# Kernel optimization log

Measured on AMD Instinct MI355X. Metric: run time of the kernel, lower is better.

## Reference

```python
import jax, jax.numpy as jnp
import numpy as np

N_EMB, D_LAT, D_HID, D_MID, D_IN = 1024, 64, 256, 128, 9
BETA = 0.25  # commitment_cost
N = 262144


def _kaiming(k, shape):
    # kaiming_normal_ with nonlinearity='relu': std = sqrt(2 / fan_in)
    fan_in = shape[1]
    return jax.random.normal(k, shape, jnp.float32) * jnp.sqrt(jnp.float32(2.0 / fan_in))


def setup_inputs() -> dict:
    key = jax.random.key(0)
    ks = jax.random.split(key, 8)
    return {
        "x": jax.random.normal(ks[0], (N, D_IN), jnp.float32),
        # Encoder: Linear(9->256) ReLU Linear(256->128) ReLU Linear(128->64)
        "enc_w1": _kaiming(ks[1], (D_HID, D_IN)),  "enc_b1": jnp.zeros((D_HID,), jnp.float32),
        "enc_w2": _kaiming(ks[2], (D_MID, D_HID)), "enc_b2": jnp.zeros((D_MID,), jnp.float32),
        "enc_w3": _kaiming(ks[3], (D_LAT, D_MID)), "enc_b3": jnp.zeros((D_LAT,), jnp.float32),
        # Decoder: Linear(64->128) ReLU Linear(128->256) ReLU Linear(256->9)
        "dec_w1": _kaiming(ks[4], (D_MID, D_LAT)), "dec_b1": jnp.zeros((D_MID,), jnp.float32),
        "dec_w2": _kaiming(ks[5], (D_HID, D_MID)), "dec_b2": jnp.zeros((D_HID,), jnp.float32),
        "dec_w3": _kaiming(ks[6], (D_IN, D_HID)),  "dec_b3": jnp.zeros((D_IN,), jnp.float32),
        # Codebook: Embedding(1024, 64), uniform(-1, 1)
        "codebook": jax.random.uniform(ks[7], (N_EMB, D_LAT), jnp.float32, -1.0, 1.0),
    }


def _mlp3(h, w1, b1, w2, b2, w3, b3):
    h = jax.nn.relu(h @ w1.T + b1)
    h = jax.nn.relu(h @ w2.T + b2)
    return h @ w3.T + b3


def reference(x, enc_w1, enc_b1, enc_w2, enc_b2, enc_w3, enc_b3,
              dec_w1, dec_b1, dec_w2, dec_b2, dec_w3, dec_b3, codebook):
    z_e = _mlp3(x, enc_w1, enc_b1, enc_w2, enc_b2, enc_w3, enc_b3)  # [N, 64]
    # squared euclidean distances to codebook: [N, N_EMB]
    d = (jnp.sum(z_e * z_e, axis=1, keepdims=True)
         - 2.0 * (z_e @ codebook.T)
         + jnp.sum(codebook * codebook, axis=1))
    idx = jnp.argmin(d, axis=1)                 # [N] int
    quantized = codebook[idx]                   # gather == onehot @ codebook
    e_latent = jnp.mean((jax.lax.stop_gradient(quantized) - z_e) ** 2)
    q_latent = jnp.mean((quantized - jax.lax.stop_gradient(z_e)) ** 2)
    vq_loss = q_latent + BETA * e_latent
    # straight-through estimator
    z_q = z_e + jax.lax.stop_gradient(quantized - z_e)
    # perplexity from codebook usage histogram (== mean of one-hot encodings)
    counts = jnp.zeros((N_EMB,), jnp.float32).at[idx].add(1.0)
    avg_probs = counts / jnp.float32(z_e.shape[0])
    perplexity = jnp.exp(-jnp.sum(avg_probs * jnp.log(avg_probs + 1e-10)))
    x_recon = _mlp3(z_q, dec_w1, dec_b1, dec_w2, dec_b2, dec_w3, dec_b3)
    return (x_recon, vq_loss, perplexity)
```

## Files before the change

kernel.cpp:

```cpp
#include <hip/hip_runtime.h>
#include <math.h>


namespace {

constexpr int kN = 262144;

typedef _Float16 half8 __attribute__((ext_vector_type(8)));
typedef float floatx4 __attribute__((ext_vector_type(4)));

#define MFMA16(a, b, c) __builtin_amdgcn_mfma_f32_16x16x32_f16((a), (b), (c), 0, 0, 0)
#define LDS_FENCE() asm volatile("s_waitcnt lgkmcnt(0)" ::: "memory")
#define VMCNT0() asm volatile("s_waitcnt vmcnt(0)" ::: "memory")
#define BARRIER()                                  \
  do {                                             \
    asm volatile("" ::: "memory");                 \
    __builtin_amdgcn_s_barrier();                  \
    asm volatile("" ::: "memory");                 \
  } while (0)

constexpr size_t W1M_O = 0;
constexpr size_t W1R_O = 16384;
constexpr size_t E2M_O = 32768;
constexpr size_t E2R_O = 98304;
constexpr size_t E3M_O = 163840;
constexpr size_t E3R_O = 180224;
constexpr size_t CBM_O = 196608;
constexpr size_t CBR_O = 327680;
constexpr size_t D1P_O = 458752;
constexpr size_t D2P_O = 475136;
constexpr size_t D3P_O = 540672;
constexpr size_t CN_O  = 548864;
constexpr size_t IDX_O = 589824;
constexpr size_t ESP_O = IDX_O + 1048576;
constexpr size_t HP_O  = ESP_O + 32768;

__device__ __forceinline__ void split2(float v, _Float16& hi, _Float16& lo) {
  hi = (_Float16)v;
  lo = (_Float16)(v - (float)hi);
}

__global__ void prep_kernel(
    const float* __restrict__ ew1, const float* __restrict__ ew2,
    const float* __restrict__ ew3, const float* __restrict__ cb,
    const float* __restrict__ dw1, const float* __restrict__ dw2,
    const float* __restrict__ dw3, char* __restrict__ wsb) {
  _Float16* w1m = (_Float16*)(wsb + W1M_O);
  _Float16* w1r = (_Float16*)(wsb + W1R_O);
  _Float16* e2m = (_Float16*)(wsb + E2M_O);
  _Float16* e2r = (_Float16*)(wsb + E2R_O);
  _Float16* e3m = (_Float16*)(wsb + E3M_O);
  _Float16* e3r = (_Float16*)(wsb + E3R_O);
  _Float16* cbm = (_Float16*)(wsb + CBM_O);
  _Float16* cbr = (_Float16*)(wsb + CBR_O);
  _Float16* d1p = (_Float16*)(wsb + D1P_O);
  _Float16* d2p = (_Float16*)(wsb + D2P_O);
  _Float16* d3p = (_Float16*)(wsb + D3P_O);
  float* cn = (float*)(wsb + CN_O);

  const int gid = blockIdx.x * 256 + threadIdx.x;
  const int stride = gridDim.x * 256;
  for (int e = gid; e < 256 * 32; e += stride) {
    int n = e >> 5, k = e & 31;
    float v = (k < 9) ? ew1[n * 9 + k] : 0.f;
    split2(v, w1m[e], w1r[e]);
  }
  for (int e = gid; e < 128 * 256; e += stride) split2(ew2[e], e2m[e], e2r[e]);
  for (int e = gid; e < 64 * 128; e += stride) split2(ew3[e], e3m[e], e3r[e]);
  for (int e = gid; e < 1024 * 64; e += stride) split2(cb[e], cbm[e], cbr[e]);
  for (int e = gid; e < 128 * 64; e += stride) d1p[e] = (_Float16)dw1[e];
  for (int e = gid; e < 256 * 128; e += stride) d2p[e] = (_Float16)dw2[e];
  for (int e = gid; e < 16 * 256; e += stride) {
    int n = e >> 8, k = e & 255;
    d3p[e] = (n < 9) ? (_Float16)dw3[n * 256 + k] : (_Float16)0.f;
  }
  for (int i = gid; i < 1024; i += stride) {
    float s = 0.f;
    const float* c = cb + (size_t)i * 64;
#pragma unroll 8
    for (int k = 0; k < 64; ++k) s = fmaf(c[k], c[k], s);
    cn[i] = s;
  }
}

__global__ __launch_bounds__(256, 3) void vqvae_mega(
    const float* __restrict__ x,
    const float* __restrict__ eb1, const float* __restrict__ eb2,
    const float* __restrict__ eb3, const float* __restrict__ db1,
    const float* __restrict__ db2, const float* __restrict__ db3,
    const float* __restrict__ cb, const char* __restrict__ wsb,
    float* __restrict__ out, int* __restrict__ idx_g, float* __restrict__ esp_g) {
  __shared__ _Float16 LP[26624];

  const int t = threadIdx.x;
  const int lane = t & 63;
  const int w = t >> 6;
  const int m = lane & 15;
  const int q = lane >> 4;
  const int R0 = blockIdx.x * 128;
  const int wr0 = 32 * w;
  _Float16* WPS = LP + 16384 + w * 2560;
  const float* cn_g = (const float*)(wsb + CN_O);
  const int swq = (m & 7) << 3;

  half8 axm[2] = {{}, {}}, axr[2] = {{}, {}};
#pragma unroll
  for (int rt = 0; rt < 2; ++rt) {
    const int grow = R0 + wr0 + 16 * rt + m;
    if (q == 0) {
#pragma unroll
      for (int j = 0; j < 8; ++j) {
        const float v = x[(size_t)grow * 9 + j];
        const _Float16 hi = (_Float16)v;
        axm[rt][j] = hi;
        axr[rt][j] = (_Float16)(v - (float)hi);
      }
    } else if (q == 1) {
      const float v = x[(size_t)grow * 9 + 8];
      const _Float16 hi = (_Float16)v;
      axm[rt][0] = hi;
      axr[rt][0] = (_Float16)(v - (float)hi);
    }
  }

  floatx4 acc2[8][2];
#pragma unroll
  for (int nt = 0; nt < 8; ++nt)
#pragma unroll
    for (int rt = 0; rt < 2; ++rt) acc2[nt][rt] = (floatx4){0.f, 0.f, 0.f, 0.f};

  {
    const int pA = t >> 7, nA = t & 127;
    const char* srcA = wsb + (pA ? E2R_O : E2M_O) + (size_t)nA * 512;
    _Float16* dstA = LP + (pA ? 5120 : 0) + nA * 40;
    half8 stg[4];
#pragma unroll
    for (int j = 0; j < 4; ++j) stg[j] = *(const half8*)(srcA + j * 16);

    for (int kc = 0; kc < 8; ++kc) {
      VMCNT0();
#pragma unroll
      for (int j = 0; j < 4; ++j) *(half8*)(dstA + j * 8) = stg[j];
      LDS_FENCE();
      if (kc < 7) {
#pragma unroll
        for (int j = 0; j < 4; ++j)
          stg[j] = *(const half8*)(srcA + (size_t)(kc + 1) * 64 + j * 16);
      }
      BARRIER();

#pragma unroll
      for (int ntl = 0; ntl < 2; ++ntl) {
        const int f = kc * 32 + ntl * 16 + m;
        const half8 bm = *(const half8*)(wsb + W1M_O + (size_t)f * 64 + q * 16);
        const half8 br = *(const half8*)(wsb + W1R_O + (size_t)f * 64 + q * 16);
        const float bias = eb1[f];
#pragma unroll
        for (int rt = 0; rt < 2; ++rt) {
          floatx4 a = (floatx4){0.f, 0.f, 0.f, 0.f};
          a = MFMA16(axr[rt], bm, a);
          a = MFMA16(axm[rt], br, a);
          a = MFMA16(axm[rt], bm, a);
#pragma unroll
          for (int reg = 0; reg < 4; ++reg) {
            const float v = fmaxf(a[reg] + bias, 0.f);
            const int row = 16 * rt + 4 * q + reg;
            const _Float16 hi = (_Float16)v;
            WPS[row * 40 + ntl * 16 + m] = hi;
            WPS[1280 + row * 40 + ntl * 16 + m] = (_Float16)(v - (float)hi);
          }
        }
      }
      LDS_FENCE();
      half8 am[2], ar[2];
#pragma unroll
      for (int rt = 0; rt < 2; ++rt) {
        am[rt] = *(const half8*)(WPS + (16 * rt + m) * 40 + q * 8);
        ar[rt] = *(const half8*)(WPS + 1280 + (16 * rt + m) * 40 + q * 8);
      }
      __builtin_amdgcn_s_setprio(1);
#pragma unroll
      for (int nt = 0; nt < 8; ++nt) {
        const half8 bm = *(const half8*)(LP + (nt * 16 + m) * 40 + q * 8);
        const half8 br = *(const half8*)(LP + 5120 + (nt * 16 + m) * 40 + q * 8);
#pragma unroll
        for (int rt = 0; rt < 2; ++rt) {
          acc2[nt][rt] = MFMA16(ar[rt], bm, acc2[nt][rt]);
          acc2[nt][rt] = MFMA16(am[rt], br, acc2[nt][rt]);
          acc2[nt][rt] = MFMA16(am[rt], bm, acc2[nt][rt]);
        }
      }
      __builtin_amdgcn_s_setprio(0);
      BARRIER();
    }
  }

  floatx4 acc3[4][2];
#pragma unroll
  for (int nt = 0; nt < 4; ++nt)
#pragma unroll
    for (int rt = 0; rt < 2; ++rt) acc3[nt][rt] = (floatx4){0.f, 0.f, 0.f, 0.f};

  for (int ks = 0; ks < 4; ++ks) {
#pragma unroll
    for (int h = 0; h < 2; ++h) {
      const int nt = 2 * ks + h;
      const float bias = eb2[nt * 16 + m];
#pragma unroll
      for (int rt = 0; rt < 2; ++rt) {
#pragma unroll
        for (int reg = 0; reg < 4; ++reg) {
          const float v = fmaxf(acc2[nt][rt][reg] + bias, 0.f);
          const int row = 16 * rt + 4 * q + reg;
          const _Float16 hi = (_Float16)v;
          WPS[row * 40 + h * 16 + m] = hi;
          WPS[1280 + row * 40 + h * 16 + m] = (_Float16)(v - (float)hi);
        }
      }
    }
    LDS_FENCE();
    half8 am[2], ar[2];
#pragma unroll
    for (int rt = 0; rt < 2; ++rt) {
      am[rt] = *(const half8*)(WPS + (16 * rt + m) * 40 + q * 8);
      ar[rt] = *(const half8*)(WPS + 1280 + (16 * rt + m) * 40 + q * 8);
    }
#pragma unroll
    for (int nt = 0; nt < 4; ++nt) {
      const half8 bm = *(const half8*)(wsb + E3M_O + (size_t)(nt * 16 + m) * 256 + ks * 64 + q * 16);
      const half8 br = *(const half8*)(wsb + E3R_O + (size_t)(nt * 16 + m) * 256 + ks * 64 + q * 16);
#pragma unroll
      for (int rt = 0; rt < 2; ++rt) {
        acc3[nt][rt] = MFMA16(ar[rt], bm, acc3[nt][rt]);
        acc3[nt][rt] = MFMA16(am[rt], br, acc3[nt][rt]);
        acc3[nt][rt] = MFMA16(am[rt], bm, acc3[nt][rt]);
      }
    }
  }

  const int pC = t >> 7, eC = t & 127;
  const int nC = eC >> 1, hC = eC & 1;
  const char* srcC = wsb + (pC ? CBR_O : CBM_O) + (size_t)nC * 128 + hC * 64;
  const int dCbase = pC * 4096 + nC * 64;
  const int swC = (nC & 7) << 3;
  half8 stgC[4];
#pragma unroll
  for (int j = 0; j < 4; ++j) stgC[j] = *(const half8*)(srcC + j * 16);

  half8 zfm[2][2], zfr[2][2];
#pragma unroll
  for (int rt = 0; rt < 2; ++rt) {
#pragma unroll
    for (int nt = 0; nt < 4; ++nt) {
      const float bias = eb3[nt * 16 + m];
#pragma unroll
      for (int reg = 0; reg < 4; ++reg) {
        const float v = acc3[nt][rt][reg] + bias;
        const int row = 4 * q + reg;
        const _Float16 hi = (_Float16)v;
        WPS[row * 72 + nt * 16 + m] = hi;
        WPS[1152 + row * 72 + nt * 16 + m] = (_Float16)(v - (float)hi);
      }
    }
    LDS_FENCE();
#pragma unroll
    for (int ks2 = 0; ks2 < 2; ++ks2) {
      zfm[rt][ks2] = *(const half8*)(WPS + m * 72 + ks2 * 32 + q * 8);
      zfr[rt][ks2] = *(const half8*)(WPS + 1152 + m * 72 + ks2 * 32 + q * 8);
    }
  }

  float bestd[2][4];
  int besti[2][4];
#pragma unroll
  for (int rt = 0; rt < 2; ++rt)
#pragma unroll
    for (int reg = 0; reg < 4; ++reg) { bestd[rt][reg] = 3.4e38f; besti[rt][reg] = 0; }

  for (int cc = 0; cc < 16; ++cc) {
    const int bb = (cc & 1) << 13;
    VMCNT0();
    {
      _Float16* d0 = LP + bb + dCbase;
#pragma unroll
      for (int j = 0; j < 4; ++j)
        *(half8*)(d0 + ((hC * 32 + j * 8) ^ swC)) = stgC[j];
    }
    LDS_FENCE();
    if (cc < 15) {
#pragma unroll
      for (int j = 0; j < 4; ++j)
        stgC[j] = *(const half8*)(srcC + (size_t)(cc + 1) * 8192 + j * 16);
    }
    BARRIER();

    floatx4 accd[4][2];
#pragma unroll
    for (int nt = 0; nt < 4; ++nt)
#pragma unroll
      for (int rt = 0; rt < 2; ++rt) accd[nt][rt] = (floatx4){0.f, 0.f, 0.f, 0.f};
    __builtin_amdgcn_s_setprio(1);
#pragma unroll
    for (int nt = 0; nt < 4; ++nt) {
#pragma unroll
      for (int ks2 = 0; ks2 < 2; ++ks2) {
        const int ko = (ks2 * 32 + q * 8) ^ swq;
        const half8 bm = *(const half8*)(LP + bb + (nt * 16 + m) * 64 + ko);
        const half8 br = *(const half8*)(LP + bb + 4096 + (nt * 16 + m) * 64 + ko);
#pragma unroll
        for (int rt = 0; rt < 2; ++rt) {
          accd[nt][rt] = MFMA16(zfr[rt][ks2], bm, accd[nt][rt]);
          accd[nt][rt] = MFMA16(zfm[rt][ks2], br, accd[nt][rt]);
          accd[nt][rt] = MFMA16(zfm[rt][ks2], bm, accd[nt][rt]);
        }
      }
    }
    __builtin_amdgcn_s_setprio(0);
#pragma unroll
    for (int nt = 0; nt < 4; ++nt) {
      const int code = cc * 64 + nt * 16 + m;
      const float cnv = cn_g[code];
#pragma unroll
      for (int rt = 0; rt < 2; ++rt) {
#pragma unroll
        for (int reg = 0; reg < 4; ++reg) {
          const float d = cnv - 2.f * accd[nt][rt][reg];
          if (d < bestd[rt][reg]) { bestd[rt][reg] = d; besti[rt][reg] = code; }
        }
      }
    }
  }
#pragma unroll
  for (int rt = 0; rt < 2; ++rt) {
#pragma unroll
    for (int reg = 0; reg < 4; ++reg) {
#pragma unroll
      for (int off = 1; off < 16; off <<= 1) {
        const float od = __shfl_xor(bestd[rt][reg], off, 16);
        const int oi = __shfl_xor(besti[rt][reg], off, 16);
        if (od < bestd[rt][reg] || (od == bestd[rt][reg] && oi < besti[rt][reg])) {
          bestd[rt][reg] = od; besti[rt][reg] = oi;
        }
      }
    }
  }
  if (m == 0) {
#pragma unroll
    for (int rt = 0; rt < 2; ++rt)
#pragma unroll
      for (int reg = 0; reg < 4; ++reg) {
        const int row = wr0 + 16 * rt + 4 * q + reg;
        idx_g[R0 + row] = besti[rt][reg];
      }
  }

  const int sl = ((m >> 2) << 4) | m;
  half8 zq[2][2];
  float es = 0.f;
#pragma unroll
  for (int rt = 0; rt < 2; ++rt) {
    const int b0 = __shfl(besti[rt][0], sl);
    const int b1 = __shfl(besti[rt][1], sl);
    const int b2 = __shfl(besti[rt][2], sl);
    const int b3 = __shfl(besti[rt][3], sl);
    const int r2 = m & 3;
    const int bi = (r2 == 0) ? b0 : (r2 == 1) ? b1 : (r2 == 2) ? b2 : b3;
#pragma unroll
    for (int ks2 = 0; ks2 < 2; ++ks2) {
      const float* cp = cb + (size_t)bi * 64 + ks2 * 32 + q * 8;
      const float4 c0 = *(const float4*)cp;
      const float4 c1 = *(const float4*)(cp + 4);
      float cv[8] = {c0.x, c0.y, c0.z, c0.w, c1.x, c1.y, c1.z, c1.w};
#pragma unroll
      for (int j = 0; j < 8; ++j) {
        const float z = (float)zfm[rt][ks2][j] + (float)zfr[rt][ks2][j];
        const float d = cv[j] - z;
        es = fmaf(d, d, es);
        zq[rt][ks2][j] = (_Float16)(z + d);
      }
    }
  }
#pragma unroll
  for (int off = 1; off < 64; off <<= 1) es += __shfl_xor(es, off, 64);
  if (lane == 0) esp_g[blockIdx.x * 4 + w] = es;

  const int nE = t >> 2, jE = t & 3;
  const char* srcE = wsb + D2P_O + (size_t)nE * 256 + jE * 64;
  const int dEbase = nE * 128;
  const int swE = (nE & 7) << 3;
  half8 stgE[4];
#pragma unroll
  for (int j = 0; j < 4; ++j) stgE[j] = *(const half8*)(srcE + j * 16);

  floatx4 accH[8][2];
#pragma unroll
  for (int nt = 0; nt < 8; ++nt)
#pragma unroll
    for (int rt = 0; rt < 2; ++rt) accH[nt][rt] = (floatx4){0.f, 0.f, 0.f, 0.f};
  __builtin_amdgcn_s_setprio(1);
#pragma unroll
  for (int nt = 0; nt < 8; ++nt) {
#pragma unroll
    for (int ks2 = 0; ks2 < 2; ++ks2) {
      const half8 b = *(const half8*)(wsb + D1P_O + (size_t)(nt * 16 + m) * 128 + ks2 * 64 + q * 16);
#pragma unroll
      for (int rt = 0; rt < 2; ++rt) accH[nt][rt] = MFMA16(zq[rt][ks2], b, accH[nt][rt]);
    }
  }
  __builtin_amdgcn_s_setprio(0);
  half8 h3f[2][4];
  for (int ks = 0; ks < 4; ++ks) {
#pragma unroll
    for (int h = 0; h < 2; ++h) {
      const int nt = 2 * ks + h;
      const float bias = db1[nt * 16 + m];
#pragma unroll
      for (int rt = 0; rt < 2; ++rt)
#pragma unroll
        for (int reg = 0; reg < 4; ++reg) {
          const float v = fmaxf(accH[nt][rt][reg] + bias, 0.f);
          WPS[(16 * rt + 4 * q + reg) * 40 + h * 16 + m] = (_Float16)v;
        }
    }
    LDS_FENCE();
#pragma unroll
    for (int rt = 0; rt < 2; ++rt)
      h3f[rt][ks] = *(const half8*)(WPS + (16 * rt + m) * 40 + q * 8);
  }

  floatx4 accO[2] = {(floatx4){0.f, 0.f, 0.f, 0.f}, (floatx4){0.f, 0.f, 0.f, 0.f}};
  for (int jc = 0; jc < 4; ++jc) {
    const int bb = (jc & 1) << 13;
    VMCNT0();
    {
      _Float16* d0 = LP + bb + dEbase;
#pragma unroll
      for (int j = 0; j < 4; ++j)
        *(half8*)(d0 + ((jE * 32 + j * 8) ^ swE)) = stgE[j];
    }
    LDS_FENCE();
    if (jc < 3) {
#pragma unroll
      for (int j = 0; j < 4; ++j)
        stgE[j] = *(const half8*)(srcE + (size_t)(jc + 1) * 16384 + j * 16);
    }
    BARRIER();

    floatx4 accD2[4][2];
#pragma unroll
    for (int nt = 0; nt < 4; ++nt)
#pragma unroll
      for (int rt = 0; rt < 2; ++rt) accD2[nt][rt] = (floatx4){0.f, 0.f, 0.f, 0.f};
    __builtin_amdgcn_s_setprio(1);
#pragma unroll
    for (int nt = 0; nt < 4; ++nt) {
#pragma unroll
      for (int ks = 0; ks < 4; ++ks) {
        const half8 b = *(const half8*)(LP + bb + (nt * 16 + m) * 128 + ((ks * 32 + q * 8) ^ swq));
#pragma unroll
        for (int rt = 0; rt < 2; ++rt) accD2[nt][rt] = MFMA16(h3f[rt][ks], b, accD2[nt][rt]);
      }
    }
    __builtin_amdgcn_s_setprio(0);
    half8 b3[2];
#pragma unroll
    for (int ks2 = 0; ks2 < 2; ++ks2)
      b3[ks2] = *(const half8*)(wsb + D3P_O + (size_t)m * 512 + jc * 128 + ks2 * 64 + q * 16);
#pragma unroll
    for (int rt = 0; rt < 2; ++rt) {
#pragma unroll
      for (int nt = 0; nt < 4; ++nt) {
        const float bias = db2[jc * 64 + nt * 16 + m];
#pragma unroll
        for (int reg = 0; reg < 4; ++reg) {
          const float v = fmaxf(accD2[nt][rt][reg] + bias, 0.f);
          WPS[(4 * q + reg) * 72 + nt * 16 + m] = (_Float16)v;
        }
      }
      LDS_FENCE();
#pragma unroll
      for (int ks2 = 0; ks2 < 2; ++ks2) {
        const half8 am = *(const half8*)(WPS + m * 72 + ks2 * 32 + q * 8);
        accO[rt] = MFMA16(am, b3[ks2], accO[rt]);
      }
    }
  }
  if (m < 9) {
    const float bias = db3[m];
#pragma unroll
    for (int rt = 0; rt < 2; ++rt)
#pragma unroll
      for (int reg = 0; reg < 4; ++reg) {
        const size_t r = (size_t)(R0 + wr0 + 16 * rt + 4 * q + reg);
        out[r * 9 + m] = accO[rt][reg] + bias;
      }
  }
}

__global__ __launch_bounds__(256) void hist_kernel(
    const int* __restrict__ idx_g, int* __restrict__ hp) {
  __shared__ int lh[1024];
  const int t = threadIdx.x;
#pragma unroll
  for (int i = 0; i < 4; ++i) lh[t * 4 + i] = 0;
  __syncthreads();
  for (int i = t; i < 4096; i += 256)
    atomicAdd(&lh[idx_g[blockIdx.x * 4096 + i]], 1);
  __syncthreads();
  int* part = hp + blockIdx.x * 1024;
#pragma unroll
  for (int i = 0; i < 4; ++i) part[t * 4 + i] = lh[t * 4 + i];
}

__global__ __launch_bounds__(1024) void finalize_kernel(
    const int* __restrict__ hp, const float* __restrict__ esp,
    float* __restrict__ out2) {
  __shared__ double red[1024];
  __shared__ float rede[1024];
  const int t = threadIdx.x;
  int h = 0;
#pragma unroll 8
  for (int p = 0; p < 64; ++p) h += hp[p * 1024 + t];
  const float pr = (float)h * (1.0f / (float)kN);
  red[t] = (double)(pr * logf(pr + 1e-10f));
  float es = 0.f;
#pragma unroll
  for (int i = 0; i < 8; ++i) es += esp[i * 1024 + t];
  rede[t] = es;
  __syncthreads();
  for (int s = 512; s > 0; s >>= 1) {
    if (t < s) { red[t] += red[t + s]; rede[t] += rede[t + s]; }
    __syncthreads();
  }
  if (t == 0) {
    out2[0] = 1.25f * (rede[0] * (1.0f / ((float)kN * 64.0f)));
    out2[1] = expf((float)(-red[0]));
  }
}

}

extern "C" void kernel_launch(void* const* d_in, const int* in_sizes, int n_in,
                              void* d_out, int out_size, void* d_ws, size_t ws_size,
                              hipStream_t stream) {
  const float* x   = (const float*)d_in[0];
  const float* ew1 = (const float*)d_in[1];
  const float* eb1 = (const float*)d_in[2];
  const float* ew2 = (const float*)d_in[3];
  const float* eb2 = (const float*)d_in[4];
  const float* ew3 = (const float*)d_in[5];
  const float* eb3 = (const float*)d_in[6];
  const float* dw1 = (const float*)d_in[7];
  const float* db1 = (const float*)d_in[8];
  const float* dw2 = (const float*)d_in[9];
  const float* db2 = (const float*)d_in[10];
  const float* dw3 = (const float*)d_in[11];
  const float* db3 = (const float*)d_in[12];
  const float* cb  = (const float*)d_in[13];
  float* out = (float*)d_out;
  char* wsb = (char*)d_ws;

  int* idx_g = (int*)(wsb + IDX_O);
  float* esp = (float*)(wsb + ESP_O);
  int* hp = (int*)(wsb + HP_O);

  prep_kernel<<<128, 256, 0, stream>>>(ew1, ew2, ew3, cb, dw1, dw2, dw3, wsb);
  vqvae_mega<<<kN / 128, 256, 0, stream>>>(x, eb1, eb2, eb3, db1, db2, db3, cb,
                                           wsb, out, idx_g, esp);
  hist_kernel<<<64, 256, 0, stream>>>(idx_g, hp);
  finalize_kernel<<<1, 1024, 0, stream>>>(hp, esp, out + (size_t)kN * 9);
}
```

Baseline: 330.4 us.

## Halve rows per block, shrink LDS with XOR swizzles, fold codebook norms into accumulator

Each wave now handles 16 rows instead of 32, so a block covers 64 rows and twice as many blocks launch. Shared memory shrinks from about 52KB to 24KB by dropping padding for XOR-swizzled layouts and single-buffering the codebook and decoder weight tiles, and the occupancy hint rises from 3 to 4 blocks. The distance search now seeds each accumulator with minus half the codebook norm and takes an argmax, which removes the per-element norm subtraction. The cost is that every block reloads the same weights and codebook for half as many rows, and single buffering adds an extra barrier per chunk.

Result: slower. 423.4 us (+28.1%).

```diff
diff --git a/kernel.cpp b/kernel.cpp
--- a/kernel.cpp
+++ b/kernel.cpp
@@ -33,7 +33,7 @@
 constexpr size_t CN_O  = 548864;
 constexpr size_t IDX_O = 589824;
 constexpr size_t ESP_O = IDX_O + 1048576;
-constexpr size_t HP_O  = ESP_O + 32768;
+constexpr size_t HP_O  = ESP_O + 65536;
 
 __device__ __forceinline__ void split2(float v, _Float16& hi, _Float16& lo) {
   hi = (_Float16)v;
@@ -83,56 +83,59 @@
   }
 }
 
-__global__ __launch_bounds__(256, 3) void vqvae_mega(
+__global__ __launch_bounds__(256, 4) void vqvae_mega(
     const float* __restrict__ x,
     const float* __restrict__ eb1, const float* __restrict__ eb2,
     const float* __restrict__ eb3, const float* __restrict__ db1,
     const float* __restrict__ db2, const float* __restrict__ db3,
     const float* __restrict__ cb, const char* __restrict__ wsb,
     float* __restrict__ out, int* __restrict__ idx_g, float* __restrict__ esp_g) {
-  __shared__ _Float16 LP[26624];
+  __shared__ _Float16 LP[12288];
 
   const int t = threadIdx.x;
   const int lane = t & 63;
   const int w = t >> 6;
   const int m = lane & 15;
   const int q = lane >> 4;
-  const int R0 = blockIdx.x * 128;
-  const int wr0 = 32 * w;
-  _Float16* WPS = LP + 16384 + w * 2560;
+  const int R0 = blockIdx.x * 64;
+  const int row0 = R0 + w * 16;
+  _Float16* WPS = LP + 8192 + w * 1024;
+  _Float16* ZT = LP + w * 2048;
   const float* cn_g = (const float*)(wsb + CN_O);
-  const int swq = (m & 7) << 3;
-
-  half8 axm[2] = {{}, {}}, axr[2] = {{}, {}};
-#pragma unroll
-  for (int rt = 0; rt < 2; ++rt) {
-    const int grow = R0 + wr0 + 16 * rt + m;
+
+  const int mh = m >> 3, ml = m & 7, m3 = m & 3, m7 = m & 7;
+  const int rA = m * 32 + ((q ^ m3) << 3);
+  const int z0 = m * 64 + (((0 * 4 + q) ^ m7) << 3);
+  const int z1 = m * 64 + (((1 * 4 + q) ^ m7) << 3);
+
+  half8 axm = {}, axr = {};
+  {
+    const int grow = row0 + m;
     if (q == 0) {
 #pragma unroll
       for (int j = 0; j < 8; ++j) {
         const float v = x[(size_t)grow * 9 + j];
         const _Float16 hi = (_Float16)v;
-        axm[rt][j] = hi;
-        axr[rt][j] = (_Float16)(v - (float)hi);
+        axm[j] = hi;
+        axr[j] = (_Float16)(v - (float)hi);
       }
     } else if (q == 1) {
       const float v = x[(size_t)grow * 9 + 8];
       const _Float16 hi = (_Float16)v;
-      axm[rt][0] = hi;
-      axr[rt][0] = (_Float16)(v - (float)hi);
-    }
-  }
-
-  floatx4 acc2[8][2];
-#pragma unroll
-  for (int nt = 0; nt < 8; ++nt)
-#pragma unroll
-    for (int rt = 0; rt < 2; ++rt) acc2[nt][rt] = (floatx4){0.f, 0.f, 0.f, 0.f};
+      axm[0] = hi;
+      axr[0] = (_Float16)(v - (float)hi);
+    }
+  }
+
+  floatx4 acc2[8];
+#pragma unroll
+  for (int nt = 0; nt < 8; ++nt) acc2[nt] = (floatx4){0.f, 0.f, 0.f, 0.f};
 
   {
     const int pA = t >> 7, nA = t & 127;
     const char* srcA = wsb + (pA ? E2R_O : E2M_O) + (size_t)nA * 512;
-    _Float16* dstA = LP + (pA ? 5120 : 0) + nA * 40;
+    _Float16* dstA = LP + pA * 4096 + nA * 32;
+    const int sA = nA & 3;
     half8 stg[4];
 #pragma unroll
     for (int j = 0; j < 4; ++j) stg[j] = *(const half8*)(srcA + j * 16);
@@ -140,7 +143,8 @@
     for (int kc = 0; kc < 8; ++kc) {
       VMCNT0();
 #pragma unroll
-      for (int j = 0; j < 4; ++j) *(half8*)(dstA + j * 8) = stg[j];
+      for (int j = 0; j < 4; ++j)
+        *(half8*)(dstA + ((j ^ sA) << 3)) = stg[j];
       LDS_FENCE();
       if (kc < 7) {
 #pragma unroll
@@ -155,51 +159,40 @@
         const half8 bm = *(const half8*)(wsb + W1M_O + (size_t)f * 64 + q * 16);
         const half8 br = *(const half8*)(wsb + W1R_O + (size_t)f * 64 + q * 16);
         const float bias = eb1[f];
-#pragma unroll
-        for (int rt = 0; rt < 2; ++rt) {
-          floatx4 a = (floatx4){0.f, 0.f, 0.f, 0.f};
-          a = MFMA16(axr[rt], bm, a);
-          a = MFMA16(axm[rt], br, a);
-          a = MFMA16(axm[rt], bm, a);
-#pragma unroll
-          for (int reg = 0; reg < 4; ++reg) {
-            const float v = fmaxf(a[reg] + bias, 0.f);
-            const int row = 16 * rt + 4 * q + reg;
-            const _Float16 hi = (_Float16)v;
-            WPS[row * 40 + ntl * 16 + m] = hi;
-            WPS[1280 + row * 40 + ntl * 16 + m] = (_Float16)(v - (float)hi);
-          }
+        floatx4 a = (floatx4){0.f, 0.f, 0.f, 0.f};
+        a = MFMA16(axr, bm, a);
+        a = MFMA16(axm, br, a);
+        a = MFMA16(axm, bm, a);
+#pragma unroll
+        for (int reg = 0; reg < 4; ++reg) {
+          const float v = fmaxf(a[reg] + bias, 0.f);
+          const int r = 4 * q + reg;
+          const int g = (ntl * 2 + mh) ^ reg;
+          const _Float16 hi = (_Float16)v;
+          WPS[r * 32 + (g << 3) + ml] = hi;
+          WPS[512 + r * 32 + (g << 3) + ml] = (_Float16)(v - (float)hi);
         }
       }
       LDS_FENCE();
-      half8 am[2], ar[2];
-#pragma unroll
-      for (int rt = 0; rt < 2; ++rt) {
-        am[rt] = *(const half8*)(WPS + (16 * rt + m) * 40 + q * 8);
-        ar[rt] = *(const half8*)(WPS + 1280 + (16 * rt + m) * 40 + q * 8);
-      }
+      const half8 am = *(const half8*)(WPS + rA);
+      const half8 ar = *(const half8*)(WPS + 512 + rA);
       __builtin_amdgcn_s_setprio(1);
 #pragma unroll
       for (int nt = 0; nt < 8; ++nt) {
-        const half8 bm = *(const half8*)(LP + (nt * 16 + m) * 40 + q * 8);
-        const half8 br = *(const half8*)(LP + 5120 + (nt * 16 + m) * 40 + q * 8);
-#pragma unroll
-        for (int rt = 0; rt < 2; ++rt) {
-          acc2[nt][rt] = MFMA16(ar[rt], bm, acc2[nt][rt]);
-          acc2[nt][rt] = MFMA16(am[rt], br, acc2[nt][rt]);
-          acc2[nt][rt] = MFMA16(am[rt], bm, acc2[nt][rt]);
-        }
+        const half8 bm = *(const half8*)(LP + nt * 512 + rA);
+        const half8 br = *(const half8*)(LP + 4096 + nt * 512 + rA);
+        acc2[nt] = MFMA16(ar, bm, acc2[nt]);
+        acc2[nt] = MFMA16(am, br, acc2[nt]);
+        acc2[nt] = MFMA16(am, bm, acc2[nt]);
       }
       __builtin_amdgcn_s_setprio(0);
       BARRIER();
     }
   }
 
-  floatx4 acc3[4][2];
-#pragma unroll
-  for (int nt = 0; nt < 4; ++nt)
-#pragma unroll
-    for (int rt = 0; rt < 2; ++rt) acc3[nt][rt] = (floatx4){0.f, 0.f, 0.f, 0.f};
+  floatx4 acc3[4];
+#pragma unroll
+  for (int nt = 0; nt < 4; ++nt) acc3[nt] = (floatx4){0.f, 0.f, 0.f, 0.f};
 
   for (int ks = 0; ks < 4; ++ks) {
 #pragma unroll
@@ -207,85 +200,68 @@
       const int nt = 2 * ks + h;
       const float bias = eb2[nt * 16 + m];
 #pragma unroll
-      for (int rt = 0; rt < 2; ++rt) {
-#pragma unroll
-        for (int reg = 0; reg < 4; ++reg) {
-          const float v = fmaxf(acc2[nt][rt][reg] + bias, 0.f);
-          const int row = 16 * rt + 4 * q + reg;
-          const _Float16 hi = (_Float16)v;
-          WPS[row * 40 + h * 16 + m] = hi;
-          WPS[1280 + row * 40 + h * 16 + m] = (_Float16)(v - (float)hi);
-        }
+      for (int reg = 0; reg < 4; ++reg) {
+        const float v = fmaxf(acc2[nt][reg] + bias, 0.f);
+        const int r = 4 * q + reg;
+        const int g = (h * 2 + mh) ^ reg;
+        const _Float16 hi = (_Float16)v;
+        WPS[r * 32 + (g << 3) + ml] = hi;
+        WPS[512 + r * 32 + (g << 3) + ml] = (_Float16)(v - (float)hi);
       }
     }
     LDS_FENCE();
-    half8 am[2], ar[2];
-#pragma unroll
-    for (int rt = 0; rt < 2; ++rt) {
-      am[rt] = *(const half8*)(WPS + (16 * rt + m) * 40 + q * 8);
-      ar[rt] = *(const half8*)(WPS + 1280 + (16 * rt + m) * 40 + q * 8);
-    }
+    const half8 am = *(const half8*)(WPS + rA);
+    const half8 ar = *(const half8*)(WPS + 512 + rA);
 #pragma unroll
     for (int nt = 0; nt < 4; ++nt) {
       const half8 bm = *(const half8*)(wsb + E3M_O + (size_t)(nt * 16 + m) * 256 + ks * 64 + q * 16);
       const half8 br = *(const half8*)(wsb + E3R_O + (size_t)(nt * 16 + m) * 256 + ks * 64 + q * 16);
-#pragma unroll
-      for (int rt = 0; rt < 2; ++rt) {
-        acc3[nt][rt] = MFMA16(ar[rt], bm, acc3[nt][rt]);
-        acc3[nt][rt] = MFMA16(am[rt], br, acc3[nt][rt]);
-        acc3[nt][rt] = MFMA16(am[rt], bm, acc3[nt][rt]);
-      }
+      acc3[nt] = MFMA16(ar, bm, acc3[nt]);
+      acc3[nt] = MFMA16(am, br, acc3[nt]);
+      acc3[nt] = MFMA16(am, bm, acc3[nt]);
     }
   }
 
   const int pC = t >> 7, eC = t & 127;
   const int nC = eC >> 1, hC = eC & 1;
   const char* srcC = wsb + (pC ? CBR_O : CBM_O) + (size_t)nC * 128 + hC * 64;
-  const int dCbase = pC * 4096 + nC * 64;
-  const int swC = (nC & 7) << 3;
+  _Float16* dstC = LP + pC * 4096 + nC * 64;
+  const int sC = nC & 7;
   half8 stgC[4];
 #pragma unroll
   for (int j = 0; j < 4; ++j) stgC[j] = *(const half8*)(srcC + j * 16);
 
-  half8 zfm[2][2], zfr[2][2];
-#pragma unroll
-  for (int rt = 0; rt < 2; ++rt) {
-#pragma unroll
-    for (int nt = 0; nt < 4; ++nt) {
-      const float bias = eb3[nt * 16 + m];
-#pragma unroll
-      for (int reg = 0; reg < 4; ++reg) {
-        const float v = acc3[nt][rt][reg] + bias;
-        const int row = 4 * q + reg;
-        const _Float16 hi = (_Float16)v;
-        WPS[row * 72 + nt * 16 + m] = hi;
-        WPS[1152 + row * 72 + nt * 16 + m] = (_Float16)(v - (float)hi);
-      }
-    }
-    LDS_FENCE();
-#pragma unroll
-    for (int ks2 = 0; ks2 < 2; ++ks2) {
-      zfm[rt][ks2] = *(const half8*)(WPS + m * 72 + ks2 * 32 + q * 8);
-      zfr[rt][ks2] = *(const half8*)(WPS + 1152 + m * 72 + ks2 * 32 + q * 8);
-    }
-  }
-
-  float bestd[2][4];
-  int besti[2][4];
-#pragma unroll
-  for (int rt = 0; rt < 2; ++rt)
-#pragma unroll
-    for (int reg = 0; reg < 4; ++reg) { bestd[rt][reg] = 3.4e38f; besti[rt][reg] = 0; }
+  half8 zfm[2], zfr[2];
+#pragma unroll
+  for (int nt = 0; nt < 4; ++nt) {
+    const float bias = eb3[nt * 16 + m];
+#pragma unroll
+    for (int reg = 0; reg < 4; ++reg) {
+      const float v = acc3[nt][reg] + bias;
+      const int r = 4 * q + reg;
+      const int g = (nt * 2 + mh) ^ (r & 7);
+      const _Float16 hi = (_Float16)v;
+      ZT[r * 64 + (g << 3) + ml] = hi;
+      ZT[1024 + r * 64 + (g << 3) + ml] = (_Float16)(v - (float)hi);
+    }
+  }
+  LDS_FENCE();
+  zfm[0] = *(const half8*)(ZT + z0);
+  zfr[0] = *(const half8*)(ZT + 1024 + z0);
+  zfm[1] = *(const half8*)(ZT + z1);
+  zfr[1] = *(const half8*)(ZT + 1024 + z1);
+  BARRIER();
+
+  float bests[4];
+  int besti[4];
+#pragma unroll
+  for (int reg = 0; reg < 4; ++reg) { bests[reg] = -3.4e38f; besti[reg] = 0; }
 
   for (int cc = 0; cc < 16; ++cc) {
-    const int bb = (cc & 1) << 13;
     VMCNT0();
-    {
-      _Float16* d0 = LP + bb + dCbase;
-#pragma unroll
-      for (int j = 0; j < 4; ++j)
-        *(half8*)(d0 + ((hC * 32 + j * 8) ^ swC)) = stgC[j];
-    }
+#pragma unroll
+    for (int j = 0; j < 4; ++j)
+      *(half8*)(dstC + (((hC * 4 + j) ^ sC) << 3)) = stgC[j];
     LDS_FENCE();
     if (cc < 15) {
 #pragma unroll
@@ -294,77 +270,65 @@
     }
     BARRIER();
 
-    floatx4 accd[4][2];
-#pragma unroll
-    for (int nt = 0; nt < 4; ++nt)
-#pragma unroll
-      for (int rt = 0; rt < 2; ++rt) accd[nt][rt] = (floatx4){0.f, 0.f, 0.f, 0.f};
+    floatx4 accd[4];
+#pragma unroll
+    for (int nt = 0; nt < 4; ++nt) {
+      const float ci = -0.5f * cn_g[cc * 64 + nt * 16 + m];
+      accd[nt] = (floatx4){ci, ci, ci, ci};
+    }
     __builtin_amdgcn_s_setprio(1);
 #pragma unroll
     for (int nt = 0; nt < 4; ++nt) {
-#pragma unroll
-      for (int ks2 = 0; ks2 < 2; ++ks2) {
-        const int ko = (ks2 * 32 + q * 8) ^ swq;
-        const half8 bm = *(const half8*)(LP + bb + (nt * 16 + m) * 64 + ko);
-        const half8 br = *(const half8*)(LP + bb + 4096 + (nt * 16 + m) * 64 + ko);
-#pragma unroll
-        for (int rt = 0; rt < 2; ++rt) {
-          accd[nt][rt] = MFMA16(zfr[rt][ks2], bm, accd[nt][rt]);
-          accd[nt][rt] = MFMA16(zfm[rt][ks2], br, accd[nt][rt]);
-          accd[nt][rt] = MFMA16(zfm[rt][ks2], bm, accd[nt][rt]);
-        }
-      }
+      const half8 bm0 = *(const half8*)(LP + nt * 1024 + z0);
+      const half8 br0 = *(const half8*)(LP + 4096 + nt * 1024 + z0);
+      accd[nt] = MFMA16(zfr[0], bm0, accd[nt]);
+      accd[nt] = MFMA16(zfm[0], br0, accd[nt]);
+      accd[nt] = MFMA16(zfm[0], bm0, accd[nt]);
+      const half8 bm1 = *(const half8*)(LP + nt * 1024 + z1);
+      const half8 br1 = *(const half8*)(LP + 4096 + nt * 1024 + z1);
+      accd[nt] = MFMA16(zfr[1], bm1, accd[nt]);
+      accd[nt] = MFMA16(zfm[1], br1, accd[nt]);
+      accd[nt] = MFMA16(zfm[1], bm1, accd[nt]);
     }
     __builtin_amdgcn_s_setprio(0);
 #pragma unroll
     for (int nt = 0; nt < 4; ++nt) {
       const int code = cc * 64 + nt * 16 + m;
-      const float cnv = cn_g[code];
-#pragma unroll
-      for (int rt = 0; rt < 2; ++rt) {
-#pragma unroll
-        for (int reg = 0; reg < 4; ++reg) {
-          const float d = cnv - 2.f * accd[nt][rt][reg];
-          if (d < bestd[rt][reg]) { bestd[rt][reg] = d; besti[rt][reg] = code; }
-        }
-      }
-    }
-  }
-#pragma unroll
-  for (int rt = 0; rt < 2; ++rt) {
-#pragma unroll
-    for (int reg = 0; reg < 4; ++reg) {
-#pragma unroll
-      for (int off = 1; off < 16; off <<= 1) {
-        const float od = __shfl_xor(bestd[rt][reg], off, 16);
-        const int oi = __shfl_xor(besti[rt][reg], off, 16);
-        if (od < bestd[rt][reg] || (od == bestd[rt][reg] && oi < besti[rt][reg])) {
-          bestd[rt][reg] = od; besti[rt][reg] = oi;
-        }
+#pragma unroll
+      for (int reg = 0; reg < 4; ++reg) {
+        const float s = accd[nt][reg];
+        if (s > bests[reg]) { bests[reg] = s; besti[reg] = code; }
+      }
+    }
+    BARRIER();
+  }
+#pragma unroll
+  for (int reg = 0; reg < 4; ++reg) {
+#pragma unroll
+    for (int off = 1; off < 16; off <<= 1) {
+      const float os = __shfl_xor(bests[reg], off, 16);
+      const int oi = __shfl_xor(besti[reg], off, 16);
+      if (os > bests[reg] || (os == bests[reg] && oi < besti[reg])) {
+        bests[reg] = os; besti[reg] = oi;
       }
     }
   }
   if (m == 0) {
 #pragma unroll
-    for (int rt = 0; rt < 2; ++rt)
-#pragma unroll
-      for (int reg = 0; reg < 4; ++reg) {
-        const int row = wr0 + 16 * rt + 4 * q + reg;
-        idx_g[R0 + row] = besti[rt][reg];
-      }
+    for (int reg = 0; reg < 4; ++reg)
+      idx_g[row0 + 4 * q + reg] = besti[reg];
   }
 
   const int sl = ((m >> 2) << 4) | m;
-  half8 zq[2][2];
+  half8 zq[2];
   float es = 0.f;
-#pragma unroll
-  for (int rt = 0; rt < 2; ++rt) {
-    const int b0 = __shfl(besti[rt][0], sl);
-    const int b1 = __shfl(besti[rt][1], sl);
-    const int b2 = __shfl(besti[rt][2], sl);
-    const int b3 = __shfl(besti[rt][3], sl);
+  {
+    const int b0 = __shfl(besti[0], sl);
+    const int b1 = __shfl(besti[1], sl);
+    const int b2 = __shfl(besti[2], sl);
+    const int b3v = __shfl(besti[3], sl);
     const int r2 = m & 3;
-    const int bi = (r2 == 0) ? b0 : (r2 == 1) ? b1 : (r2 == 2) ? b2 : b3;
+    const int bi = (r2 == 0) ? b0 : (r2 == 1) ? b1 : (r2 == 2) ? b2 : b3v;
 #pragma unroll
     for (int ks2 = 0; ks2 < 2; ++ks2) {
       const float* cp = cb + (size_t)bi * 64 + ks2 * 32 + q * 8;
@@ -373,10 +337,10 @@
       float cv[8] = {c0.x, c0.y, c0.z, c0.w, c1.x, c1.y, c1.z, c1.w};
 #pragma unroll
       for (int j = 0; j < 8; ++j) {
-        const float z = (float)zfm[rt][ks2][j] + (float)zfr[rt][ks2][j];
+        const float z = (float)zfm[ks2][j] + (float)zfr[ks2][j];
         const float d = cv[j] - z;
         es = fmaf(d, d, es);
-        zq[rt][ks2][j] = (_Float16)(z + d);
+        zq[ks2][j] = (_Float16)(z + d);
       }
     }
   }
@@ -386,58 +350,49 @@
 
   const int nE = t >> 2, jE = t & 3;
   const char* srcE = wsb + D2P_O + (size_t)nE * 256 + jE * 64;
-  const int dEbase = nE * 128;
-  const int swE = (nE & 7) << 3;
+  _Float16* dstE = LP + nE * 128;
+  const int sE = nE & 15;
   half8 stgE[4];
 #pragma unroll
   for (int j = 0; j < 4; ++j) stgE[j] = *(const half8*)(srcE + j * 16);
 
-  floatx4 accH[8][2];
-#pragma unroll
-  for (int nt = 0; nt < 8; ++nt)
-#pragma unroll
-    for (int rt = 0; rt < 2; ++rt) accH[nt][rt] = (floatx4){0.f, 0.f, 0.f, 0.f};
+  floatx4 accH[8];
+#pragma unroll
+  for (int nt = 0; nt < 8; ++nt) accH[nt] = (floatx4){0.f, 0.f, 0.f, 0.f};
   __builtin_amdgcn_s_setprio(1);
 #pragma unroll
   for (int nt = 0; nt < 8; ++nt) {
 #pragma unroll
     for (int ks2 = 0; ks2 < 2; ++ks2) {
       const half8 b = *(const half8*)(wsb + D1P_O + (size_t)(nt * 16 + m) * 128 + ks2 * 64 + q * 16);
-#pragma unroll
-      for (int rt = 0; rt < 2; ++rt) accH[nt][rt] = MFMA16(zq[rt][ks2], b, accH[nt][rt]);
+      accH[nt] = MFMA16(zq[ks2], b, accH[nt]);
     }
   }
   __builtin_amdgcn_s_setprio(0);
-  half8 h3f[2][4];
+  half8 h3f[4];
   for (int ks = 0; ks < 4; ++ks) {
 #pragma unroll
     for (int h = 0; h < 2; ++h) {
       const int nt = 2 * ks + h;
       const float bias = db1[nt * 16 + m];
 #pragma unroll
-      for (int rt = 0; rt < 2; ++rt)
-#pragma unroll
-        for (int reg = 0; reg < 4; ++reg) {
-          const float v = fmaxf(accH[nt][rt][reg] + bias, 0.f);
-          WPS[(16 * rt + 4 * q + reg) * 40 + h * 16 + m] = (_Float16)v;
-        }
+      for (int reg = 0; reg < 4; ++reg) {
+        const float v = fmaxf(accH[nt][reg] + bias, 0.f);
+        const int r = 4 * q + reg;
+        const int g = (h * 2 + mh) ^ reg;
+        WPS[r * 32 + (g << 3) + ml] = (_Float16)v;
+      }
     }
     LDS_FENCE();
-#pragma unroll
-    for (int rt = 0; rt < 2; ++rt)
-      h3f[rt][ks] = *(const half8*)(WPS + (16 * rt + m) * 40 + q * 8);
-  }
-
-  floatx4 accO[2] = {(floatx4){0.f, 0.f, 0.f, 0.f}, (floatx4){0.f, 0.f, 0.f, 0.f}};
+    h3f[ks] = *(const half8*)(WPS + rA);
+  }
+
+  floatx4 accO = (floatx4){0.f, 0.f, 0.f, 0.f};
   for (int jc = 0; jc < 4; ++jc) {
-    const int bb = (jc & 1) << 13;
     VMCNT0();
-    {
-      _Float16* d0 = LP + bb + dEbase;
-#pragma unroll
-      for (int j = 0; j < 4; ++j)
-        *(half8*)(d0 + ((jE * 32 + j * 8) ^ swE)) = stgE[j];
-    }
+#pragma unroll
+    for (int j = 0; j < 4; ++j)
+      *(half8*)(dstE + (((jE * 4 + j) ^ sE) << 3)) = stgE[j];
     LDS_FENCE();
     if (jc < 3) {
 #pragma unroll
@@ -446,19 +401,17 @@
     }
     BARRIER();
 
-    floatx4 accD2[4][2];
-#pragma unroll
-    for (int nt = 0; nt < 4; ++nt)
-#pragma unroll
-      for (int rt = 0; rt < 2; ++rt) accD2[nt][rt] = (floatx4){0.f, 0.f, 0.f, 0.f};
+    floatx4 accD2[4];
+#pragma unroll
+    for (int nt = 0; nt < 4; ++nt) accD2[nt] = (floatx4){0.f, 0.f, 0.f, 0.f};
     __builtin_amdgcn_s_setprio(1);
 #pragma unroll
     for (int nt = 0; nt < 4; ++nt) {
+      const int n2 = nt * 16 + m;
 #pragma unroll
       for (int ks = 0; ks < 4; ++ks) {
-        const half8 b = *(const half8*)(LP + bb + (nt * 16 + m) * 128 + ((ks * 32 + q * 8) ^ swq));
-#pragma unroll
-        for (int rt = 0; rt < 2; ++rt) accD2[nt][rt] = MFMA16(h3f[rt][ks], b, accD2[nt][rt]);
+        const half8 b = *(const half8*)(LP + n2 * 128 + (((ks * 4 + q) ^ m) << 3));
+        accD2[nt] = MFMA16(h3f[ks], b, accD2[nt]);
       }
     }
     __builtin_amdgcn_s_setprio(0);
@@ -467,33 +420,32 @@
     for (int ks2 = 0; ks2 < 2; ++ks2)
       b3[ks2] = *(const half8*)(wsb + D3P_O + (size_t)m * 512 + jc * 128 + ks2 * 64 + q * 16);
 #pragma unroll
-    for (int rt = 0; rt < 2; ++rt) {
-#pragma unroll
-      for (int nt = 0; nt < 4; ++nt) {
-        const float bias = db2[jc * 64 + nt * 16 + m];
-#pragma unroll
-        for (int reg = 0; reg < 4; ++reg) {
-          const float v = fmaxf(accD2[nt][rt][reg] + bias, 0.f);
-          WPS[(4 * q + reg) * 72 + nt * 16 + m] = (_Float16)v;
-        }
-      }
-      LDS_FENCE();
-#pragma unroll
-      for (int ks2 = 0; ks2 < 2; ++ks2) {
-        const half8 am = *(const half8*)(WPS + m * 72 + ks2 * 32 + q * 8);
-        accO[rt] = MFMA16(am, b3[ks2], accO[rt]);
-      }
-    }
+    for (int nt = 0; nt < 4; ++nt) {
+      const float bias = db2[jc * 64 + nt * 16 + m];
+#pragma unroll
+      for (int reg = 0; reg < 4; ++reg) {
+        const float v = fmaxf(accD2[nt][reg] + bias, 0.f);
+        const int r = 4 * q + reg;
+        const int g = (nt * 2 + mh) ^ (r & 7);
+        WPS[r * 64 + (g << 3) + ml] = (_Float16)v;
+      }
+    }
+    LDS_FENCE();
+    {
+      const half8 a0 = *(const half8*)(WPS + z0);
+      accO = MFMA16(a0, b3[0], accO);
+      const half8 a1 = *(const half8*)(WPS + z1);
+      accO = MFMA16(a1, b3[1], accO);
+    }
+    BARRIER();
   }
   if (m < 9) {
     const float bias = db3[m];
 #pragma unroll
-    for (int rt = 0; rt < 2; ++rt)
-#pragma unroll
-      for (int reg = 0; reg < 4; ++reg) {
-        const size_t r = (size_t)(R0 + wr0 + 16 * rt + 4 * q + reg);
-        out[r * 9 + m] = accO[rt][reg] + bias;
-      }
+    for (int reg = 0; reg < 4; ++reg) {
+      const size_t r = (size_t)(row0 + 4 * q + reg);
+      out[r * 9 + m] = accO[reg] + bias;
+    }
   }
 }
 
@@ -525,7 +477,7 @@
   red[t] = (double)(pr * logf(pr + 1e-10f));
   float es = 0.f;
 #pragma unroll
-  for (int i = 0; i < 8; ++i) es += esp[i * 1024 + t];
+  for (int i = 0; i < 16; ++i) es += esp[i * 1024 + t];
   rede[t] = es;
   __syncthreads();
   for (int s = 512; s > 0; s >>= 1) {
@@ -565,8 +517,8 @@
   int* hp = (int*)(wsb + HP_O);
 
   prep_kernel<<<128, 256, 0, stream>>>(ew1, ew2, ew3, cb, dw1, dw2, dw3, wsb);
-  vqvae_mega<<<kN / 128, 256, 0, stream>>>(x, eb1, eb2, eb3, db1, db2, db3, cb,
-                                           wsb, out, idx_g, esp);
+  vqvae_mega<<<kN / 64, 256, 0, stream>>>(x, eb1, eb2, eb3, db1, db2, db3, cb,
+                                          wsb, out, idx_g, esp);
   hist_kernel<<<64, 256, 0, stream>>>(idx_g, hp);
   finalize_kernel<<<1, 1024, 0, stream>>>(hp, esp, out + (size_t)kN * 9);
 }
```
